# Performance work log

Measured on AMD Instinct MI355X. Metric: run time of the kernel, lower is better.

Reference implementation:

```python
import jax, jax.numpy as jnp
import numpy as np


def _pdists(X):
    # Pairwise Euclidean distances (torch.cdist, p=2) via the Gram trick.
    sq = jnp.sum(X * X, axis=1)                      # (bs,)
    d2 = sq[:, None] + sq[None, :] - 2.0 * (X @ X.T)  # (bs, bs)
    d2 = jnp.maximum(d2, 0.0)
    # safe sqrt: exact forward, finite gradient at 0
    pos = d2 > 0
    return jnp.where(pos, jnp.sqrt(jnp.where(pos, d2, 1.0)), 0.0)


def setup_inputs() -> dict:
    key = jax.random.key(0)
    k1, k2, k3 = jax.random.split(key, 3)
    bs, d = 4096, 512
    n_classes, n_domains = 4, 3
    X = jax.random.normal(k1, (bs, d), dtype=jnp.float32)
    ds = jax.random.randint(k2, (bs,), 0, n_domains, dtype=jnp.int64 if jax.config.read('jax_enable_x64') else jnp.int32)
    y = jax.random.randint(k3, (bs,), 0, n_classes, dtype=jnp.int64 if jax.config.read('jax_enable_x64') else jnp.int32)
    return {"X": X, "ds": ds, "y": y, "n_classes": n_classes, "n_domains": n_domains}


def reference(X, ds, y, n_classes, n_domains):
    # Equivalent to JointCCSA.LSA / JointCCSA.LS with norm=True, assuming every
    # class and domain value appears in the batch (what torch.unique would find).
    dists = _pdists(X)                                # (bs, bs)

    d_lt = ds[:, None] < ds[None, :]                  # domain pair (d1 < d2) ordering
    same_y = y[:, None] == y[None, :]
    y_lt = y[:, None] < y[None, :]                    # class pair (c1 < c2) ordering

    # SA loss: 0.5 * sum over (i,j) with y_i==y_j, ds_i<ds_j
    sa_loss = 0.5 * jnp.sum(jnp.where(same_y & d_lt, dists, 0.0))
    n_sa = n_classes * (n_domains * (n_domains - 1) // 2)
    sa_loss = sa_loss / n_sa

    # S loss: hinge on margin=1, 0.5 * sum over (i,j) with y_i<y_j, ds_i<ds_j
    margin = 1.0
    h = jnp.maximum(0.0, margin - dists)
    s_loss = 0.5 * jnp.sum(jnp.where(y_lt & d_lt, h, 0.0))
    n_s = (n_classes * (n_classes - 1) // 2) * (n_domains * (n_domains - 1) // 2)
    s_loss = s_loss / n_s

    return sa_loss, s_loss
```

## Files before the change

kernel.cpp:

```cpp
#include <hip/hip_runtime.h>
#include <hip/hip_bf16.h>
#include <stdint.h>

#define NROW 4096
#define DIM  512
#define BM   128
#define BN   128
#define BKE  128
#define NKT  (DIM / BKE)
#define PANEL_KT (BM * BKE)

typedef __attribute__((ext_vector_type(4))) float floatx4;

typedef const __attribute__((address_space(1))) void gvoid_t;
typedef __attribute__((address_space(3))) void       svoid_t;

__global__ __launch_bounds__(256) void prep_kernel(
    const float* __restrict__ X, const int* __restrict__ ds,
    const int* __restrict__ y, unsigned char* __restrict__ Xq,
    float2* __restrict__ meta, float* __restrict__ out)
{
    const int wave = threadIdx.x >> 6;
    const int lane = threadIdx.x & 63;
    const int row  = blockIdx.x * 4 + wave;
    const float4* xr = (const float4*)(X + (size_t)row * DIM);
    float4 v0 = xr[2 * lane];
    float4 v1 = xr[2 * lane + 1];
    float s = v0.x*v0.x + v0.y*v0.y + v0.z*v0.z + v0.w*v0.w
            + v1.x*v1.x + v1.y*v1.y + v1.z*v1.z + v1.w*v1.w;
    int q0 = __builtin_amdgcn_cvt_pk_fp8_f32(v0.x, v0.y, 0, false);
    q0     = __builtin_amdgcn_cvt_pk_fp8_f32(v0.z, v0.w, q0, true);
    int q1 = __builtin_amdgcn_cvt_pk_fp8_f32(v1.x, v1.y, 0, false);
    q1     = __builtin_amdgcn_cvt_pk_fp8_f32(v1.z, v1.w, q1, true);
    const int g8  = row >> 3;
    const int l3r = row & 7;
    const int kt  = lane >> 4;
    const int c   = lane & 15;
    const int p8  = c ^ (row & 15);
    *(uint2*)(Xq + ((size_t)(kt * 512 + g8) * 8 + l3r) * 128 + p8 * 8) =
        make_uint2((unsigned)q0, (unsigned)q1);
    #pragma unroll
    for (int off = 32; off; off >>= 1) s += __shfl_xor(s, off);
    if (lane == 0)
        meta[row] = make_float2(s, __int_as_float(y[row] * 4 + ds[row]));
    if (blockIdx.x == 0 && threadIdx.x < 2) out[threadIdx.x] = 0.0f;
}

__global__ __launch_bounds__(512, 4) void ccsa_kernel(
    const unsigned char* __restrict__ Xq, const float2* __restrict__ meta,
    const int* __restrict__ ncls, const int* __restrict__ ndom,
    float* __restrict__ out)
{
    __shared__ __align__(16) unsigned char As[2 * PANEL_KT];
    __shared__ __align__(16) unsigned char Bs[2 * PANEL_KT];
    __shared__ float red[16];

    const int t = blockIdx.x;
    int r = (int)((sqrtf(8.0f * (float)t + 1.0f) - 1.0f) * 0.5f);
    while ((r + 1) * (r + 2) / 2 <= t) ++r;
    while (r * (r + 1) / 2 > t) --r;
    const int bj_t = r;
    const int bi_t = t - r * (r + 1) / 2;
    const bool diag = (bi_t == bj_t);
    const int bm0 = bi_t * BM;
    const int bn0 = bj_t * BN;
    const int GA = bm0 >> 3;
    const int GB = bn0 >> 3;

    const int tid    = threadIdx.x;
    const int wave   = tid >> 6;
    const int lane   = tid & 63;
    const int warp_m = wave >> 2;
    const int warp_n = wave & 3;
    const int m15    = lane & 15;
    const int quad   = lane >> 4;

    float sqj[2]; int yj[2], dj[2];
    #pragma unroll
    for (int tn = 0; tn < 2; ++tn) {
        const float2 mj = meta[bn0 + warp_n * 32 + tn * 16 + m15];
        sqj[tn] = mj.x;
        const int ydj = __float_as_int(mj.y);
        dj[tn] = ydj & 3; yj[tn] = ydj >> 2;
    }

    floatx4 acc[4][2];
    #pragma unroll
    for (int a = 0; a < 4; ++a)
        #pragma unroll
        for (int b = 0; b < 2; ++b)
            acc[a][b] = (floatx4){0.f, 0.f, 0.f, 0.f};

    const unsigned char* Bb = diag ? As : Bs;

    #define STAGE(buf, kt)                                                    \
        do {                                                                  \
            const unsigned char* srcA =                                       \
                Xq + (size_t)((kt) * 512 + GA) * 1024;                        \
            __builtin_amdgcn_global_load_lds(                                 \
                (gvoid_t*)(srcA + tid * 16),                                  \
                (svoid_t*)(&As[(buf) * PANEL_KT + tid * 16]), 16, 0, 0);      \
            __builtin_amdgcn_global_load_lds(                                 \
                (gvoid_t*)(srcA + 8192 + tid * 16),                           \
                (svoid_t*)(&As[(buf) * PANEL_KT + 8192 + tid * 16]),          \
                16, 0, 0);                                                    \
            if (!diag) {                                                      \
                const unsigned char* srcB =                                   \
                    Xq + (size_t)((kt) * 512 + GB) * 1024;                    \
                __builtin_amdgcn_global_load_lds(                             \
                    (gvoid_t*)(srcB + tid * 16),                              \
                    (svoid_t*)(&Bs[(buf) * PANEL_KT + tid * 16]), 16, 0, 0);  \
                __builtin_amdgcn_global_load_lds(                             \
                    (gvoid_t*)(srcB + 8192 + tid * 16),                       \
                    (svoid_t*)(&Bs[(buf) * PANEL_KT + 8192 + tid * 16]),      \
                    16, 0, 0);                                                \
            }                                                                 \
        } while (0)

    const int rla0 = (warp_m * 64 +  0 + m15) * 128;
    const int rla1 = (warp_m * 64 + 16 + m15) * 128;
    const int rla2 = (warp_m * 64 + 32 + m15) * 128;
    const int rla3 = (warp_m * 64 + 48 + m15) * 128;
    const int rlb0 = (warp_n * 32 +  0 + m15) * 128;
    const int rlb1 = (warp_n * 32 + 16 + m15) * 128;

    STAGE(0, 0);
    for (int kt = 0; kt < NKT; ++kt) {
        const int cur = kt & 1;
        __syncthreads();
        if (kt + 1 < NKT) STAGE(cur ^ 1, kt + 1);
        const int cb = cur * PANEL_KT;

        #pragma unroll
        for (int s = 0; s < 4; ++s) {
            const int ph = ((s * 4 + quad) ^ m15) * 8;
            const long a0 = *(const long*)(&As[cb + rla0 + ph]);
            const long a1 = *(const long*)(&As[cb + rla1 + ph]);
            const long a2 = *(const long*)(&As[cb + rla2 + ph]);
            const long a3 = *(const long*)(&As[cb + rla3 + ph]);
            const long b0 = *(const long*)(&Bb[cb + rlb0 + ph]);
            const long b1 = *(const long*)(&Bb[cb + rlb1 + ph]);
            acc[0][0] = __builtin_amdgcn_mfma_f32_16x16x32_fp8_fp8(a0, b0, acc[0][0], 0, 0, 0);
            acc[0][1] = __builtin_amdgcn_mfma_f32_16x16x32_fp8_fp8(a0, b1, acc[0][1], 0, 0, 0);
            acc[1][0] = __builtin_amdgcn_mfma_f32_16x16x32_fp8_fp8(a1, b0, acc[1][0], 0, 0, 0);
            acc[1][1] = __builtin_amdgcn_mfma_f32_16x16x32_fp8_fp8(a1, b1, acc[1][1], 0, 0, 0);
            acc[2][0] = __builtin_amdgcn_mfma_f32_16x16x32_fp8_fp8(a2, b0, acc[2][0], 0, 0, 0);
            acc[2][1] = __builtin_amdgcn_mfma_f32_16x16x32_fp8_fp8(a2, b1, acc[2][1], 0, 0, 0);
            acc[3][0] = __builtin_amdgcn_mfma_f32_16x16x32_fp8_fp8(a3, b0, acc[3][0], 0, 0, 0);
            acc[3][1] = __builtin_amdgcn_mfma_f32_16x16x32_fp8_fp8(a3, b1, acc[3][1], 0, 0, 0);
        }
    }
    #undef STAGE

    float sa = 0.f, ss = 0.f;
    #pragma unroll
    for (int tm = 0; tm < 4; ++tm) {
        #pragma unroll
        for (int rr = 0; rr < 4; ++rr) {
            const int i = bm0 + warp_m * 64 + tm * 16 + quad * 4 + rr;
            const float2 mi = meta[i];
            const int ydi = __float_as_int(mi.y);
            const int di = ydi & 3, yi = ydi >> 2;
            #pragma unroll
            for (int tn = 0; tn < 2; ++tn) {
                if (diag) {
                    if (di < dj[tn]) {
                        const float d2   = mi.x + sqj[tn] - 2.0f * acc[tm][tn][rr];
                        const float dist = sqrtf(fmaxf(d2, 0.f));
                        if (yi == yj[tn])     sa += dist;
                        else if (yi < yj[tn]) ss += fmaxf(0.f, 1.f - dist);
                    }
                } else {
                    if (di != dj[tn]) {
                        const float d2   = mi.x + sqj[tn] - 2.0f * acc[tm][tn][rr];
                        const float dist = sqrtf(fmaxf(d2, 0.f));
                        if (yi == yj[tn]) {
                            sa += dist;
                        } else {
                            const bool take = (di < dj[tn]) ? (yi < yj[tn])
                                                            : (yj[tn] < yi);
                            if (take) ss += fmaxf(0.f, 1.f - dist);
                        }
                    }
                }
            }
        }
    }
    #pragma unroll
    for (int off = 32; off; off >>= 1) {
        sa += __shfl_xor(sa, off);
        ss += __shfl_xor(ss, off);
    }
    if (lane == 0) { red[wave] = sa; red[8 + wave] = ss; }
    __syncthreads();
    if (tid == 0) {
        float tsa = 0.f, tss = 0.f;
        #pragma unroll
        for (int w = 0; w < 8; ++w) { tsa += red[w]; tss += red[8 + w]; }
        const int nc = *ncls, nd = *ndom;
        const float n_sa = (float)(nc * (nd * (nd - 1) / 2));
        const float n_s  = (float)((nc * (nc - 1) / 2) * (nd * (nd - 1) / 2));
        atomicAdd(out + 0, tsa * 0.5f / n_sa);
        atomicAdd(out + 1, tss * 0.5f / n_s);
    }
}

extern "C" void kernel_launch(void* const* d_in, const int* in_sizes, int n_in,
                              void* d_out, int out_size, void* d_ws, size_t ws_size,
                              hipStream_t stream) {
    (void)in_sizes; (void)n_in; (void)out_size; (void)ws_size;
    const float* X  = (const float*)d_in[0];
    const int*   ds = (const int*)d_in[1];
    const int*   y  = (const int*)d_in[2];
    const int*   nc = (const int*)d_in[3];
    const int*   nd = (const int*)d_in[4];
    float* out = (float*)d_out;

    unsigned char* Xq = (unsigned char*)d_ws;
    float2* meta = (float2*)((char*)d_ws + (size_t)NROW * DIM);

    prep_kernel<<<NROW / 4, 256, 0, stream>>>(X, ds, y, Xq, meta, out);
    const int ntiles = NROW / BM;
    const int nblocks = ntiles * (ntiles + 1) / 2;
    ccsa_kernel<<<nblocks, 512, 0, stream>>>(Xq, meta, nc, nd, out);
}
```

Measured before the change: 97.34 us.

## Use 4-wave blocks with 64x64 warp tiles and 64-wide K panels

The GEMM block drops from 8 waves to 4, and each wave now computes a 64x64 sub-tile (4x4 MFMAs) instead of 64x32, which raises register-level operand reuse. The K panel shrinks from 128 to 64 bytes, so the fp8 layout written by the prep kernel and its XOR swizzle are changed to match, and LDS use per block is halved. The costs are fewer waves per block to hide latency, more accumulator registers per thread, and twice as many K iterations and barriers.

```diff
diff --git a/kernel.cpp b/kernel.cpp
--- a/kernel.cpp
+++ b/kernel.cpp
@@ -6,7 +6,7 @@
 #define DIM  512
 #define BM   128
 #define BN   128
-#define BKE  128
+#define BKE  64
 #define NKT  (DIM / BKE)
 #define PANEL_KT (BM * BKE)
 
@@ -32,13 +32,11 @@
     q0     = __builtin_amdgcn_cvt_pk_fp8_f32(v0.z, v0.w, q0, true);
     int q1 = __builtin_amdgcn_cvt_pk_fp8_f32(v1.x, v1.y, 0, false);
     q1     = __builtin_amdgcn_cvt_pk_fp8_f32(v1.z, v1.w, q1, true);
-    const int g8  = row >> 3;
-    const int l3r = row & 7;
-    const int kt  = lane >> 4;
-    const int c   = lane & 15;
-    const int p8  = c ^ (row & 15);
-    *(uint2*)(Xq + ((size_t)(kt * 512 + g8) * 8 + l3r) * 128 + p8 * 8) =
-        make_uint2((unsigned)q0, (unsigned)q1);
+    const int kt = lane >> 3;
+    const int c  = lane & 7;
+    const int p  = c ^ (row & 7);
+    *(uint2*)(Xq + ((size_t)(kt * 512 + (row >> 3)) * 8 + (row & 7)) * 64
+              + p * 8) = make_uint2((unsigned)q0, (unsigned)q1);
     #pragma unroll
     for (int off = 32; off; off >>= 1) s += __shfl_xor(s, off);
     if (lane == 0)
@@ -46,14 +44,14 @@
     if (blockIdx.x == 0 && threadIdx.x < 2) out[threadIdx.x] = 0.0f;
 }
 
-__global__ __launch_bounds__(512, 4) void ccsa_kernel(
+__global__ __launch_bounds__(256, 4) void ccsa_kernel(
     const unsigned char* __restrict__ Xq, const float2* __restrict__ meta,
     const int* __restrict__ ncls, const int* __restrict__ ndom,
     float* __restrict__ out)
 {
     __shared__ __align__(16) unsigned char As[2 * PANEL_KT];
     __shared__ __align__(16) unsigned char Bs[2 * PANEL_KT];
-    __shared__ float red[16];
+    __shared__ float red[8];
 
     const int t = blockIdx.x;
     int r = (int)((sqrtf(8.0f * (float)t + 1.0f) - 1.0f) * 0.5f);
@@ -70,25 +68,26 @@
     const int tid    = threadIdx.x;
     const int wave   = tid >> 6;
     const int lane   = tid & 63;
-    const int warp_m = wave >> 2;
-    const int warp_n = wave & 3;
+    const int warp_m = wave >> 1;
+    const int warp_n = wave & 1;
     const int m15    = lane & 15;
     const int quad   = lane >> 4;
-
-    float sqj[2]; int yj[2], dj[2];
-    #pragma unroll
-    for (int tn = 0; tn < 2; ++tn) {
-        const float2 mj = meta[bn0 + warp_n * 32 + tn * 16 + m15];
+    const int sw     = m15 & 7;
+
+    float sqj[4]; int yj[4], dj[4];
+    #pragma unroll
+    for (int tn = 0; tn < 4; ++tn) {
+        const float2 mj = meta[bn0 + warp_n * 64 + tn * 16 + m15];
         sqj[tn] = mj.x;
         const int ydj = __float_as_int(mj.y);
         dj[tn] = ydj & 3; yj[tn] = ydj >> 2;
     }
 
-    floatx4 acc[4][2];
+    floatx4 acc[4][4];
     #pragma unroll
     for (int a = 0; a < 4; ++a)
         #pragma unroll
-        for (int b = 0; b < 2; ++b)
+        for (int b = 0; b < 4; ++b)
             acc[a][b] = (floatx4){0.f, 0.f, 0.f, 0.f};
 
     const unsigned char* Bb = diag ? As : Bs;
@@ -96,33 +95,35 @@
     #define STAGE(buf, kt)                                                    \
         do {                                                                  \
             const unsigned char* srcA =                                       \
-                Xq + (size_t)((kt) * 512 + GA) * 1024;                        \
+                Xq + (size_t)((kt) * 512 + GA) * 512;                         \
             __builtin_amdgcn_global_load_lds(                                 \
                 (gvoid_t*)(srcA + tid * 16),                                  \
                 (svoid_t*)(&As[(buf) * PANEL_KT + tid * 16]), 16, 0, 0);      \
             __builtin_amdgcn_global_load_lds(                                 \
-                (gvoid_t*)(srcA + 8192 + tid * 16),                           \
-                (svoid_t*)(&As[(buf) * PANEL_KT + 8192 + tid * 16]),          \
+                (gvoid_t*)(srcA + 4096 + tid * 16),                           \
+                (svoid_t*)(&As[(buf) * PANEL_KT + 4096 + tid * 16]),          \
                 16, 0, 0);                                                    \
             if (!diag) {                                                      \
                 const unsigned char* srcB =                                   \
-                    Xq + (size_t)((kt) * 512 + GB) * 1024;                    \
+                    Xq + (size_t)((kt) * 512 + GB) * 512;                     \
                 __builtin_amdgcn_global_load_lds(                             \
                     (gvoid_t*)(srcB + tid * 16),                              \
                     (svoid_t*)(&Bs[(buf) * PANEL_KT + tid * 16]), 16, 0, 0);  \
                 __builtin_amdgcn_global_load_lds(                             \
-                    (gvoid_t*)(srcB + 8192 + tid * 16),                       \
-                    (svoid_t*)(&Bs[(buf) * PANEL_KT + 8192 + tid * 16]),      \
+                    (gvoid_t*)(srcB + 4096 + tid * 16),                       \
+                    (svoid_t*)(&Bs[(buf) * PANEL_KT + 4096 + tid * 16]),      \
                     16, 0, 0);                                                \
             }                                                                 \
         } while (0)
 
-    const int rla0 = (warp_m * 64 +  0 + m15) * 128;
-    const int rla1 = (warp_m * 64 + 16 + m15) * 128;
-    const int rla2 = (warp_m * 64 + 32 + m15) * 128;
-    const int rla3 = (warp_m * 64 + 48 + m15) * 128;
-    const int rlb0 = (warp_n * 32 +  0 + m15) * 128;
-    const int rlb1 = (warp_n * 32 + 16 + m15) * 128;
+    int offA[4], offB[4];
+    #pragma unroll
+    for (int tt = 0; tt < 4; ++tt) {
+        const int rla = warp_m * 64 + tt * 16 + m15;
+        const int rlb = warp_n * 64 + tt * 16 + m15;
+        offA[tt] = (rla >> 3) * 512 + (rla & 7) * 64;
+        offB[tt] = (rlb >> 3) * 512 + (rlb & 7) * 64;
+    }
 
     STAGE(0, 0);
     for (int kt = 0; kt < NKT; ++kt) {
@@ -132,22 +133,20 @@
         const int cb = cur * PANEL_KT;
 
         #pragma unroll
-        for (int s = 0; s < 4; ++s) {
-            const int ph = ((s * 4 + quad) ^ m15) * 8;
-            const long a0 = *(const long*)(&As[cb + rla0 + ph]);
-            const long a1 = *(const long*)(&As[cb + rla1 + ph]);
-            const long a2 = *(const long*)(&As[cb + rla2 + ph]);
-            const long a3 = *(const long*)(&As[cb + rla3 + ph]);
-            const long b0 = *(const long*)(&Bb[cb + rlb0 + ph]);
-            const long b1 = *(const long*)(&Bb[cb + rlb1 + ph]);
-            acc[0][0] = __builtin_amdgcn_mfma_f32_16x16x32_fp8_fp8(a0, b0, acc[0][0], 0, 0, 0);
-            acc[0][1] = __builtin_amdgcn_mfma_f32_16x16x32_fp8_fp8(a0, b1, acc[0][1], 0, 0, 0);
-            acc[1][0] = __builtin_amdgcn_mfma_f32_16x16x32_fp8_fp8(a1, b0, acc[1][0], 0, 0, 0);
-            acc[1][1] = __builtin_amdgcn_mfma_f32_16x16x32_fp8_fp8(a1, b1, acc[1][1], 0, 0, 0);
-            acc[2][0] = __builtin_amdgcn_mfma_f32_16x16x32_fp8_fp8(a2, b0, acc[2][0], 0, 0, 0);
-            acc[2][1] = __builtin_amdgcn_mfma_f32_16x16x32_fp8_fp8(a2, b1, acc[2][1], 0, 0, 0);
-            acc[3][0] = __builtin_amdgcn_mfma_f32_16x16x32_fp8_fp8(a3, b0, acc[3][0], 0, 0, 0);
-            acc[3][1] = __builtin_amdgcn_mfma_f32_16x16x32_fp8_fp8(a3, b1, acc[3][1], 0, 0, 0);
+        for (int s = 0; s < 2; ++s) {
+            const int ph = ((s * 4 + quad) ^ sw) * 8;
+            long a[4], b[4];
+            #pragma unroll
+            for (int tt = 0; tt < 4; ++tt) {
+                a[tt] = *(const long*)(&As[cb + offA[tt] + ph]);
+                b[tt] = *(const long*)(&Bb[cb + offB[tt] + ph]);
+            }
+            #pragma unroll
+            for (int tm = 0; tm < 4; ++tm)
+                #pragma unroll
+                for (int tn = 0; tn < 4; ++tn)
+                    acc[tm][tn] = __builtin_amdgcn_mfma_f32_16x16x32_fp8_fp8(
+                        a[tm], b[tn], acc[tm][tn], 0, 0, 0);
         }
     }
     #undef STAGE
@@ -162,7 +161,7 @@
             const int ydi = __float_as_int(mi.y);
             const int di = ydi & 3, yi = ydi >> 2;
             #pragma unroll
-            for (int tn = 0; tn < 2; ++tn) {
+            for (int tn = 0; tn < 4; ++tn) {
                 if (diag) {
                     if (di < dj[tn]) {
                         const float d2   = mi.x + sqj[tn] - 2.0f * acc[tm][tn][rr];
@@ -191,12 +190,11 @@
         sa += __shfl_xor(sa, off);
         ss += __shfl_xor(ss, off);
     }
-    if (lane == 0) { red[wave] = sa; red[8 + wave] = ss; }
+    if (lane == 0) { red[wave] = sa; red[4 + wave] = ss; }
     __syncthreads();
     if (tid == 0) {
-        float tsa = 0.f, tss = 0.f;
-        #pragma unroll
-        for (int w = 0; w < 8; ++w) { tsa += red[w]; tss += red[8 + w]; }
+        const float tsa = red[0] + red[1] + red[2] + red[3];
+        const float tss = red[4] + red[5] + red[6] + red[7];
         const int nc = *ncls, nd = *ndom;
         const float n_sa = (float)(nc * (nd * (nd - 1) / 2));
         const float n_s  = (float)((nc * (nc - 1) / 2) * (nd * (nd - 1) / 2));
@@ -222,5 +220,5 @@
     prep_kernel<<<NROW / 4, 256, 0, stream>>>(X, ds, y, Xq, meta, out);
     const int ntiles = NROW / BM;
     const int nblocks = ntiles * (ntiles + 1) / 2;
-    ccsa_kernel<<<nblocks, 512, 0, stream>>>(Xq, meta, nc, nd, out);
+    ccsa_kernel<<<nblocks, 256, 0, stream>>>(Xq, meta, nc, nd, out);
 }
```

New measurement: 99.17 us. No clear change (+1.9%).

## Sort rows by domain and skip same-domain tiles in pairwise kernel

Applied to the files above, without the earlier changes.

Adds a setup kernel that histograms domain ids. The prep kernel then scatters the quantized rows and their metadata into domain-sorted order using atomic counters. The main kernel skips any 128x128 tile whose rows and columns all belong to one domain, since those pairs never contribute to either loss. It also permutes the block order with a stride-97 mapping to spread the remaining work across the GPU. The cost is an extra serial single-block launch, and row order inside each domain is nondeterministic, which may change floating-point summation order.

```diff
diff --git a/kernel.cpp b/kernel.cpp
--- a/kernel.cpp
+++ b/kernel.cpp
@@ -9,20 +9,52 @@
 #define BKE  128
 #define NKT  (DIM / BKE)
 #define PANEL_KT (BM * BKE)
+#define NTILES (NROW / BM)
+#define NBLK  (NTILES * (NTILES + 1) / 2)
 
 typedef __attribute__((ext_vector_type(4))) float floatx4;
 
 typedef const __attribute__((address_space(1))) void gvoid_t;
 typedef __attribute__((address_space(3))) void       svoid_t;
+
+__global__ __launch_bounds__(256) void setup_kernel(
+    const int* __restrict__ ds, int* __restrict__ ctrl,
+    float* __restrict__ out)
+{
+    __shared__ int hist[3];
+    const int tid = threadIdx.x;
+    if (tid < 3) hist[tid] = 0;
+    __syncthreads();
+    int c0 = 0, c1 = 0, c2 = 0;
+    for (int i = tid; i < NROW; i += 256) {
+        const int d = ds[i];
+        c0 += (d == 0); c1 += (d == 1); c2 += (d == 2);
+    }
+    if (c0) atomicAdd(&hist[0], c0);
+    if (c1) atomicAdd(&hist[1], c1);
+    if (c2) atomicAdd(&hist[2], c2);
+    __syncthreads();
+    if (tid == 0) {
+        const int n0 = hist[0], n1 = hist[1];
+        ctrl[0] = 0; ctrl[1] = n0; ctrl[2] = n0 + n1; ctrl[3] = NROW;
+        ctrl[4] = 0; ctrl[5] = n0; ctrl[6] = n0 + n1;
+        out[0] = 0.f; out[1] = 0.f;
+    }
+}
 
 __global__ __launch_bounds__(256) void prep_kernel(
     const float* __restrict__ X, const int* __restrict__ ds,
     const int* __restrict__ y, unsigned char* __restrict__ Xq,
-    float2* __restrict__ meta, float* __restrict__ out)
+    float2* __restrict__ meta, int* __restrict__ ctrl)
 {
     const int wave = threadIdx.x >> 6;
     const int lane = threadIdx.x & 63;
     const int row  = blockIdx.x * 4 + wave;
+    const int d    = ds[row];
+    int nr0 = 0;
+    if (lane == 0) nr0 = atomicAdd(&ctrl[4 + d], 1);
+    const int nr = __shfl(nr0, 0);
+
     const float4* xr = (const float4*)(X + (size_t)row * DIM);
     float4 v0 = xr[2 * lane];
     float4 v1 = xr[2 * lane + 1];
@@ -32,22 +64,20 @@
     q0     = __builtin_amdgcn_cvt_pk_fp8_f32(v0.z, v0.w, q0, true);
     int q1 = __builtin_amdgcn_cvt_pk_fp8_f32(v1.x, v1.y, 0, false);
     q1     = __builtin_amdgcn_cvt_pk_fp8_f32(v1.z, v1.w, q1, true);
-    const int g8  = row >> 3;
-    const int l3r = row & 7;
-    const int kt  = lane >> 4;
-    const int c   = lane & 15;
-    const int p8  = c ^ (row & 15);
-    *(uint2*)(Xq + ((size_t)(kt * 512 + g8) * 8 + l3r) * 128 + p8 * 8) =
-        make_uint2((unsigned)q0, (unsigned)q1);
+    const int kt = lane >> 4;
+    const int c  = lane & 15;
+    const int p8 = c ^ (nr & 15);
+    *(uint2*)(Xq + ((size_t)(kt * 512 + (nr >> 3)) * 8 + (nr & 7)) * 128
+              + p8 * 8) = make_uint2((unsigned)q0, (unsigned)q1);
     #pragma unroll
     for (int off = 32; off; off >>= 1) s += __shfl_xor(s, off);
     if (lane == 0)
-        meta[row] = make_float2(s, __int_as_float(y[row] * 4 + ds[row]));
-    if (blockIdx.x == 0 && threadIdx.x < 2) out[threadIdx.x] = 0.0f;
+        meta[nr] = make_float2(s, __int_as_float(y[row] * 4 + d));
 }
 
 __global__ __launch_bounds__(512, 4) void ccsa_kernel(
     const unsigned char* __restrict__ Xq, const float2* __restrict__ meta,
+    const int* __restrict__ ctrl,
     const int* __restrict__ ncls, const int* __restrict__ ndom,
     float* __restrict__ out)
 {
@@ -55,7 +85,7 @@
     __shared__ __align__(16) unsigned char Bs[2 * PANEL_KT];
     __shared__ float red[16];
 
-    const int t = blockIdx.x;
+    const int t = (blockIdx.x * 97) % NBLK;
     int r = (int)((sqrtf(8.0f * (float)t + 1.0f) - 1.0f) * 0.5f);
     while ((r + 1) * (r + 2) / 2 <= t) ++r;
     while (r * (r + 1) / 2 > t) --r;
@@ -64,6 +94,19 @@
     const bool diag = (bi_t == bj_t);
     const int bm0 = bi_t * BM;
     const int bn0 = bj_t * BN;
+
+    {
+        const int b1 = ctrl[1], b2 = ctrl[2];
+        int domr = -1, domc = -2;
+        if (bm0 + BM <= b1) domr = 0;
+        else if (bm0 >= b1 && bm0 + BM <= b2) domr = 1;
+        else if (bm0 >= b2) domr = 2;
+        if (bn0 + BN <= b1) domc = 0;
+        else if (bn0 >= b1 && bn0 + BN <= b2) domc = 1;
+        else if (bn0 >= b2) domc = 2;
+        if (domr >= 0 && domr == domc) return;
+    }
+
     const int GA = bm0 >> 3;
     const int GB = bn0 >> 3;
 
@@ -218,9 +261,9 @@
 
     unsigned char* Xq = (unsigned char*)d_ws;
     float2* meta = (float2*)((char*)d_ws + (size_t)NROW * DIM);
-
-    prep_kernel<<<NROW / 4, 256, 0, stream>>>(X, ds, y, Xq, meta, out);
-    const int ntiles = NROW / BM;
-    const int nblocks = ntiles * (ntiles + 1) / 2;
-    ccsa_kernel<<<nblocks, 512, 0, stream>>>(Xq, meta, nc, nd, out);
-}
+    int* ctrl = (int*)((char*)d_ws + (size_t)NROW * DIM + NROW * 8);
+
+    setup_kernel<<<1, 256, 0, stream>>>(ds, ctrl, out);
+    prep_kernel<<<NROW / 4, 256, 0, stream>>>(X, ds, y, Xq, meta, ctrl);
+    ccsa_kernel<<<NBLK, 512, 0, stream>>>(Xq, meta, ctrl, nc, nd, out);
+}
```

Measured after the change: 141.9 us. +45.8%, slower.
